# Kernel optimization log

Hardware: AMD Instinct MI355X
Metric: run time of the kernel (lower is better)

The kernel has to match this reference:

```python
import jax, jax.numpy as jnp
import numpy as np

LN_EPS = 1e-5
NEG_INF = -1e38

def _layer_norm(x, g, b):
    mu = x.mean(-1, keepdims=True)
    var = ((x - mu) ** 2).mean(-1, keepdims=True)
    return (x - mu) * jax.lax.rsqrt(var + LN_EPS) * g + b

def _wkv(w, u, k, v):
    # w,u: [C]; k,v: [B,T,C]. Numerically-stable RWKV WKV scan over T.
    B, T, C = k.shape
    kt = jnp.swapaxes(k, 0, 1)  # [T,B,C]
    vt = jnp.swapaxes(v, 0, 1)
    aa0 = jnp.zeros((B, C), k.dtype)
    bb0 = jnp.zeros((B, C), k.dtype)
    pp0 = jnp.full((B, C), NEG_INF, k.dtype)

    def step(carry, inp):
        aa, bb, pp = carry
        kk, vv = inp
        p = jnp.maximum(pp, u + kk)
        e1 = jnp.exp(pp - p)
        e2 = jnp.exp(u + kk - p)
        y = (e1 * aa + e2 * vv) / (e1 + e2)
        p2 = jnp.maximum(pp + w, w + kk)
        e1u = jnp.exp(pp + w - p2)
        e2u = jnp.exp(w + kk - p2)
        aa2 = e1u * aa + e2u * vv
        bb2 = e1u + e2u
        pp2 = p2 + jnp.log(bb2)
        return (aa2, bb2, pp2), y

    _, ys = jax.lax.scan(step, (aa0, bb0, pp0), (kt, vt))
    return jnp.swapaxes(ys, 0, 1)  # [B,T,C]

def _shift(h):
    # x_prev: zero-pad one step at the front (state=None path)
    return jnp.pad(h[:, :-1, :], ((0, 0), (1, 0), (0, 0)))

def setup_inputs() -> dict:
    key = jax.random.key(0)
    B, T, C = 8, 2048, 1024
    ks = jax.random.split(key, 12)
    s = 0.02
    return {
        "x": jax.random.normal(ks[0], (B, T, C), jnp.float32),
        "time_decay": jax.random.normal(ks[1], (C,), jnp.float32) * 0.01,
        "time_first": jax.random.normal(ks[2], (C,), jnp.float32) * 0.01,
        "w_tk": jax.random.normal(ks[3], (C, C), jnp.float32) * s,
        "w_tv": jax.random.normal(ks[4], (C, C), jnp.float32) * s,
        "w_tr": jax.random.normal(ks[5], (C, C), jnp.float32) * s,
        "w_ck": jax.random.normal(ks[6], (C, 4 * C), jnp.float32) * s,
        "w_cv": jax.random.normal(ks[7], (4 * C, C), jnp.float32) * s,
        "w_cr": jax.random.normal(ks[8], (C, C), jnp.float32) * s,
        "ln1_g": jnp.ones((C,), jnp.float32),
        "ln1_b": jnp.zeros((C,), jnp.float32),
        "ln2_g": jnp.ones((C,), jnp.float32),
        "ln2_b": jnp.zeros((C,), jnp.float32),
        "mix_k": jnp.ones((1, 1, C), jnp.float32),
        "mix_v": jnp.ones((1, 1, C), jnp.float32),
        "mix_r": jnp.ones((1, 1, C), jnp.float32),
        "cmix_k": jnp.ones((1, 1, C), jnp.float32),
        "cmix_r": jnp.ones((1, 1, C), jnp.float32),
    }

def reference(x, time_decay, time_first, w_tk, w_tv, w_tr, w_ck, w_cv, w_cr,
              ln1_g, ln1_b, ln2_g, ln2_b, mix_k, mix_v, mix_r, cmix_k, cmix_r):
    # --- time mixing (residual branch 1); dropout is identity at eval ---
    h = _layer_norm(x, ln1_g, ln1_b)
    hp = _shift(h)
    xk = h * mix_k + hp * (1.0 - mix_k)
    xv = h * mix_v + hp * (1.0 - mix_v)
    xr = h * mix_r + hp * (1.0 - mix_r)
    k = xk @ w_tk
    v = xv @ w_tv
    r = jax.nn.sigmoid(xr @ w_tr)
    y = _wkv(time_decay, time_first, k, v)
    x = x + r * y
    # --- channel mixing (residual branch 2) ---
    h2 = _layer_norm(x, ln2_g, ln2_b)
    hp2 = _shift(h2)
    ck = h2 * cmix_k + hp2 * (1.0 - cmix_k)
    cr = h2 * cmix_r + hp2 * (1.0 - cmix_r)
    kk = jnp.square(jax.nn.relu(ck @ w_ck))  # [B,T,4C]
    x = x + jax.nn.sigmoid(cr @ w_cr) * (kk @ w_cv)
    return x
```

## Files before the change

kernel.cpp:

```cpp
#include <hip/hip_runtime.h>
#include <hip/hip_bf16.h>
#include <stdint.h>

#define LN_EPS 1e-5f
#define LNR 8

typedef __attribute__((ext_vector_type(8))) __bf16 bf16x8;
typedef __attribute__((ext_vector_type(8))) short short8;
typedef __attribute__((ext_vector_type(4))) float floatx4;

__device__ __forceinline__ ushort f2bf(float f) {
    __hip_bfloat16 h = __float2bfloat16(f);
    return *reinterpret_cast<ushort*>(&h);
}
__device__ __forceinline__ float bf2f(ushort u) {
    return __builtin_bit_cast(float, ((unsigned int)u) << 16);
}

__device__ __forceinline__ void gload16(const void* g, void* l) {
#if __has_builtin(__builtin_amdgcn_global_load_lds)
    __builtin_amdgcn_global_load_lds(
        (const __attribute__((address_space(1))) unsigned int*)g,
        (__attribute__((address_space(3))) unsigned int*)l, 16, 0, 0);
#else
    *(int4*)l = *(const int4*)g;
#endif
}

#define SBAR __builtin_amdgcn_s_barrier()
#define SCHED0 __builtin_amdgcn_sched_barrier(0)
#define WAIT_LGKM0 asm volatile("s_waitcnt lgkmcnt(0)" ::: "memory")
#define WAIT_VM4 asm volatile("s_waitcnt vmcnt(4)" ::: "memory")
#define WAIT_VM0 asm volatile("s_waitcnt vmcnt(0)" ::: "memory")

#define STAGE_A(h, t)                                                        \
    do {                                                                     \
        ushort* _d = &lds[((((t) & 1) * 2 + 0) * 2 + (h)) * 8192];           \
        const long _o = (long)(h) * 128 * lda + (long)(t) * 64;              \
        gload16(aS0 + _o, _d + tid * 8);                                     \
        gload16(aS1 + _o, _d + (tid + 512) * 8);                             \
    } while (0)
#define STAGE_B(h, t)                                                        \
    do {                                                                     \
        ushort* _d = &lds[((((t) & 1) * 2 + 1) * 2 + (h)) * 8192];           \
        const long _o = (long)(h) * 128 * ldb + (long)(t) * 64;              \
        gload16(bS0 + _o, _d + tid * 8);                                     \
        gload16(bS1 + _o, _d + (tid + 512) * 8);                             \
    } while (0)
#define GEMM_LDA(MB)                                                         \
    _Pragma("unroll") for (int mi = 0; mi < 4; ++mi)                         \
    _Pragma("unroll") for (int ks = 0; ks < 2; ++ks)                         \
        a[mi][ks] = __builtin_bit_cast(                                      \
            bf16x8, *(const short8*)&ldsA[((MB) + mi) * 1024 + ks * 512 + aoff]);
#define GEMM_LDB(NB)                                                         \
    _Pragma("unroll") for (int ni = 0; ni < 2; ++ni)                         \
    _Pragma("unroll") for (int ks = 0; ks < 2; ++ks)                         \
        b[(NB) + ni][ks] = __builtin_bit_cast(                               \
            bf16x8, *(const short8*)&ldsB[((NB) + ni) * 1024 + ks * 512 + boff]);
#define GEMM_MFMA(MB, NB)                                                    \
    __builtin_amdgcn_s_setprio(1);                                           \
    _Pragma("unroll") for (int mi = 0; mi < 4; ++mi)                         \
    _Pragma("unroll") for (int ni = 0; ni < 2; ++ni)                         \
    _Pragma("unroll") for (int ks = 0; ks < 2; ++ks)                         \
        acc[(MB) + mi][(NB) + ni] = __builtin_amdgcn_mfma_f32_16x16x32_bf16( \
            a[mi][ks], b[(NB) + ni][ks], acc[(MB) + mi][(NB) + ni], 0, 0, 0);\
    __builtin_amdgcn_s_setprio(0);

template <int EPI>
__global__ __launch_bounds__(512, 2) void gemm256(
    const ushort* __restrict__ A, const ushort* __restrict__ Bt,
    int K, int lda, int ldb, int ldc,
    float* __restrict__ outF, ushort* __restrict__ outB,
    const float* __restrict__ add0, const ushort* __restrict__ mul0) {
    extern __shared__ ushort lds[];

    const int tid  = threadIdx.x;
    const int lane = tid & 63;
    const int quad = lane >> 4;
    const int l16  = lane & 15;
    const int wv   = tid >> 6;
    const int wmi  = wv >> 2;
    const int wni  = wv & 3;

    const int gx  = gridDim.x;
    const int nwg = gx * gridDim.y;
    int b_ = blockIdx.y * gx + blockIdx.x;
    b_ = (b_ & 7) * (nwg >> 3) + (b_ >> 3);
    const long m0 = (long)(b_ / gx) * 256;
    const long n0 = (long)(b_ % gx) * 256;

    floatx4 acc[8][4];
#pragma unroll
    for (int i = 0; i < 8; ++i)
#pragma unroll
        for (int j = 0; j < 4; ++j) acc[i][j] = (floatx4)0.f;

    const int j1 = tid + 512;
    const int r0 = ((tid >> 7) << 4) + (tid & 15);
    const int c0 = (tid >> 4) & 7;
    const int col0 = (c0 & 3) * 8 + (c0 >> 2) * 32;
    const int r1 = ((j1 >> 7) << 4) + (j1 & 15);
    const int c1 = (j1 >> 4) & 7;
    const int col1 = (c1 & 3) * 8 + (c1 >> 2) * 32;
    const ushort* aS0 = A + (m0 + r0) * (long)lda + col0;
    const ushort* aS1 = A + (m0 + r1) * (long)lda + col1;
    const ushort* bS0 = Bt + (n0 + r0) * (long)ldb + col0;
    const ushort* bS1 = Bt + (n0 + r1) * (long)ldb + col1;

    const int aoff = quad * 128 + l16 * 8;
    const int boff = (wni & 1) * 4096 + quad * 128 + l16 * 8;

    const int NT = K >> 6;

    STAGE_A(0, 0); STAGE_A(1, 0);
    STAGE_B(0, 0); STAGE_B(1, 0);
    if (NT > 1) { STAGE_B(0, 1); STAGE_B(1, 1); WAIT_VM4; }
    else        { WAIT_VM0; }
    SBAR;

    bf16x8 a[4][2], b[4][2];
    for (int kt = 0; kt < NT; ++kt) {
        const int d = kt & 1;
        const ushort* ldsA = &lds[((d * 2 + 0) * 2 + wmi) * 8192];
        const ushort* ldsB = &lds[((d * 2 + 1) * 2 + (wni >> 1)) * 8192];

        GEMM_LDA(0)
        GEMM_LDB(0)
        GEMM_LDB(2)
        if (kt + 1 < NT) { STAGE_A(0, kt + 1); STAGE_A(1, kt + 1); }
        SBAR; WAIT_LGKM0; SCHED0;
        GEMM_MFMA(0, 0)
        GEMM_MFMA(0, 2)
        SCHED0; SBAR;

        GEMM_LDA(4)
        if (kt + 2 < NT) { STAGE_B(0, kt + 2); STAGE_B(1, kt + 2); }
        SBAR; WAIT_LGKM0; SCHED0;
        GEMM_MFMA(4, 0)
        GEMM_MFMA(4, 2)
        SCHED0;
        if (kt < NT - 2) { WAIT_VM4; } else { WAIT_VM0; }
        SBAR;
    }

#pragma unroll
    for (int mi = 0; mi < 8; ++mi) {
#pragma unroll
        for (int ni = 0; ni < 4; ++ni) {
            const long n = n0 + wni * 64 + ni * 16 + l16;
#pragma unroll
            for (int r = 0; r < 4; ++r) {
                const long m = m0 + wmi * 128 + mi * 16 + quad * 4 + r;
                const long idx = m * (long)ldc + n;
                float v = acc[mi][ni][r];
                if constexpr (EPI == 0) {
                    outB[idx] = f2bf(v);
                } else if constexpr (EPI == 1) {
                    outB[idx] = f2bf(1.f / (1.f + __expf(-v)));
                } else if constexpr (EPI == 2) {
                    float t = fmaxf(v, 0.f);
                    outB[idx] = f2bf(t * t);
                } else if constexpr (EPI == 3) {
                    outF[idx] = add0[idx] + bf2f(mul0[idx]) * v;
                }
            }
        }
    }
}

__global__ __launch_bounds__(256) void ln_mix3_b(
    const float* __restrict__ x, const float* __restrict__ g,
    const float* __restrict__ be,
    const float* __restrict__ mx0, const float* __restrict__ mx1,
    const float* __restrict__ mx2,
    ushort* __restrict__ o0, ushort* __restrict__ o1, ushort* __restrict__ o2,
    int T, int C) {
    const long r0 = (long)blockIdx.x * LNR;
    const int tid = threadIdx.x;
    const int i0 = tid * 4;
    const int wv = tid >> 6;
    __shared__ float part[2][4][2];

    const floatx4 gv  = *(const floatx4*)&g[i0];
    const floatx4 bv  = *(const floatx4*)&be[i0];
    const floatx4 mk0 = *(const floatx4*)&mx0[i0];
    const floatx4 mk1 = *(const floatx4*)&mx1[i0];
    const floatx4 mk2 = *(const floatx4*)&mx2[i0];
    const float invC = 1.f / (float)C;

    floatx4 hp = (floatx4)0.f;
    if ((int)(r0 % T) != 0) {
        floatx4 xp = *(const floatx4*)&x[(r0 - 1) * C + i0];
        float s = xp.x + xp.y + xp.z + xp.w;
        float q = xp.x * xp.x + xp.y * xp.y + xp.z * xp.z + xp.w * xp.w;
#pragma unroll
        for (int off = 32; off; off >>= 1) {
            s += __shfl_xor(s, off); q += __shfl_xor(q, off);
        }
        if ((tid & 63) == 0) { part[0][wv][0] = s; part[0][wv][1] = q; }
        __syncthreads();
        s = part[0][0][0] + part[0][1][0] + part[0][2][0] + part[0][3][0];
        q = part[0][0][1] + part[0][1][1] + part[0][2][1] + part[0][3][1];
        float mu = s * invC;
        float rs = rsqrtf(q * invC - mu * mu + LN_EPS);
        hp = (xp - mu) * rs * gv + bv;
        __syncthreads();
    }

    for (int r = 0; r < LNR; ++r) {
        const long row = r0 + r;
        floatx4 xc = *(const floatx4*)&x[row * C + i0];
        float s = xc.x + xc.y + xc.z + xc.w;
        float q = xc.x * xc.x + xc.y * xc.y + xc.z * xc.z + xc.w * xc.w;
#pragma unroll
        for (int off = 32; off; off >>= 1) {
            s += __shfl_xor(s, off); q += __shfl_xor(q, off);
        }
        const int pb = r & 1;
        if ((tid & 63) == 0) { part[pb][wv][0] = s; part[pb][wv][1] = q; }
        __syncthreads();
        s = part[pb][0][0] + part[pb][1][0] + part[pb][2][0] + part[pb][3][0];
        q = part[pb][0][1] + part[pb][1][1] + part[pb][2][1] + part[pb][3][1];
        float mu = s * invC;
        float rs = rsqrtf(q * invC - mu * mu + LN_EPS);
        floatx4 hc = (xc - mu) * rs * gv + bv;

        {
            floatx4 v = hc * mk0 + hp * (1.f - mk0);
            ushort4 pk;
            pk.x = f2bf(v.x); pk.y = f2bf(v.y); pk.z = f2bf(v.z); pk.w = f2bf(v.w);
            *(ushort4*)&o0[row * C + i0] = pk;
        }
        {
            floatx4 v = hc * mk1 + hp * (1.f - mk1);
            ushort4 pk;
            pk.x = f2bf(v.x); pk.y = f2bf(v.y); pk.z = f2bf(v.z); pk.w = f2bf(v.w);
            *(ushort4*)&o1[row * C + i0] = pk;
        }
        {
            floatx4 v = hc * mk2 + hp * (1.f - mk2);
            ushort4 pk;
            pk.x = f2bf(v.x); pk.y = f2bf(v.y); pk.z = f2bf(v.z); pk.w = f2bf(v.w);
            *(ushort4*)&o2[row * C + i0] = pk;
        }
        hp = hc;
    }
}

__global__ __launch_bounds__(256) void ln_mix_add_b(
    const float* __restrict__ x, const ushort* __restrict__ ry,
    const float* __restrict__ g, const float* __restrict__ be,
    const float* __restrict__ mx0, const float* __restrict__ mx1,
    float* __restrict__ outx,
    ushort* __restrict__ o0, ushort* __restrict__ o1, int T, int C) {
    const long r0 = (long)blockIdx.x * LNR;
    const int tid = threadIdx.x;
    const int i0 = tid * 4;
    const int wv = tid >> 6;
    __shared__ float part[2][4][2];

    const floatx4 gv  = *(const floatx4*)&g[i0];
    const floatx4 bv  = *(const floatx4*)&be[i0];
    const floatx4 mk0 = *(const floatx4*)&mx0[i0];
    const floatx4 mk1 = *(const floatx4*)&mx1[i0];
    const float invC = 1.f / (float)C;

    floatx4 hp = (floatx4)0.f;
    if ((int)(r0 % T) != 0) {
        floatx4 xp = *(const floatx4*)&x[(r0 - 1) * C + i0];
        ushort4 rp = *(const ushort4*)&ry[(r0 - 1) * C + i0];
        xp.x += bf2f(rp.x); xp.y += bf2f(rp.y); xp.z += bf2f(rp.z); xp.w += bf2f(rp.w);
        float s = xp.x + xp.y + xp.z + xp.w;
        float q = xp.x * xp.x + xp.y * xp.y + xp.z * xp.z + xp.w * xp.w;
#pragma unroll
        for (int off = 32; off; off >>= 1) {
            s += __shfl_xor(s, off); q += __shfl_xor(q, off);
        }
        if ((tid & 63) == 0) { part[0][wv][0] = s; part[0][wv][1] = q; }
        __syncthreads();
        s = part[0][0][0] + part[0][1][0] + part[0][2][0] + part[0][3][0];
        q = part[0][0][1] + part[0][1][1] + part[0][2][1] + part[0][3][1];
        float mu = s * invC;
        float rs = rsqrtf(q * invC - mu * mu + LN_EPS);
        hp = (xp - mu) * rs * gv + bv;
        __syncthreads();
    }

    for (int r = 0; r < LNR; ++r) {
        const long row = r0 + r;
        floatx4 xc = *(const floatx4*)&x[row * C + i0];
        ushort4 rc = *(const ushort4*)&ry[row * C + i0];
        xc.x += bf2f(rc.x); xc.y += bf2f(rc.y); xc.z += bf2f(rc.z); xc.w += bf2f(rc.w);
        *(floatx4*)&outx[row * C + i0] = xc;

        float s = xc.x + xc.y + xc.z + xc.w;
        float q = xc.x * xc.x + xc.y * xc.y + xc.z * xc.z + xc.w * xc.w;
#pragma unroll
        for (int off = 32; off; off >>= 1) {
            s += __shfl_xor(s, off); q += __shfl_xor(q, off);
        }
        const int pb = r & 1;
        if ((tid & 63) == 0) { part[pb][wv][0] = s; part[pb][wv][1] = q; }
        __syncthreads();
        s = part[pb][0][0] + part[pb][1][0] + part[pb][2][0] + part[pb][3][0];
        q = part[pb][0][1] + part[pb][1][1] + part[pb][2][1] + part[pb][3][1];
        float mu = s * invC;
        float rs = rsqrtf(q * invC - mu * mu + LN_EPS);
        floatx4 hc = (xc - mu) * rs * gv + bv;

        {
            floatx4 v = hc * mk0 + hp * (1.f - mk0);
            ushort4 pk;
            pk.x = f2bf(v.x); pk.y = f2bf(v.y); pk.z = f2bf(v.z); pk.w = f2bf(v.w);
            *(ushort4*)&o0[row * C + i0] = pk;
        }
        {
            floatx4 v = hc * mk1 + hp * (1.f - mk1);
            ushort4 pk;
            pk.x = f2bf(v.x); pk.y = f2bf(v.y); pk.z = f2bf(v.z); pk.w = f2bf(v.w);
            *(ushort4*)&o1[row * C + i0] = pk;
        }
        hp = hc;
    }
}


__global__ __launch_bounds__(256) void wkv_pp_local(
    const float* __restrict__ w, const ushort* __restrict__ k,
    float* __restrict__ pp_loc, int C, int L) {
    const int g = blockIdx.x * 256 + threadIdx.x;
    const int c = g % C;
    const long seg = g / C;
    const float L2E = 1.4426950408889634f;
    const float w2 = w[c] * L2E;
    const ushort* kp = k + seg * L * C + c;
    float pp = -1e38f;
    for (int j = 0; j < L; ++j) {
        float kk = bf2f(kp[(long)j * C]) * L2E;
        float ppw = pp + w2;
        float wk = w2 + kk;
        float p2 = fmaxf(ppw, wk);
        pp = p2 + log2f(exp2f(ppw - p2) + exp2f(wk - p2));
    }
    pp_loc[g] = pp;
}

__global__ __launch_bounds__(256) void wkv_pp_compose(
    const float* __restrict__ w, const float* __restrict__ pp_loc,
    float* __restrict__ pp_in, int C, int SEG, int L) {
    const int g = blockIdx.x * 256 + threadIdx.x;
    const int c = g % C;
    const long b = g / C;
    const float wL = w[c] * 1.4426950408889634f * (float)L;
    float pp = -1e38f;
    for (int s = 0; s < SEG; ++s) {
        const long idx = (b * SEG + s) * C + c;
        pp_in[idx] = pp;
        float lhs = pp + wL;
        float rhs = pp_loc[idx];
        float m = fmaxf(lhs, rhs);
        pp = m + log2f(exp2f(lhs - m) + exp2f(rhs - m));
    }
}

__global__ __launch_bounds__(256) void wkv_ab_local(
    const float* __restrict__ w, const ushort* __restrict__ k,
    const ushort* __restrict__ v, const float* __restrict__ pp_in,
    float* __restrict__ alpha, float* __restrict__ beta, int C, int L) {
    const int g = blockIdx.x * 256 + threadIdx.x;
    const int c = g % C;
    const long seg = g / C;
    const float L2E = 1.4426950408889634f;
    const float w2 = w[c] * L2E;
    const ushort* kp = k + seg * L * C + c;
    const ushort* vp = v + seg * L * C + c;
    float pp = pp_in[g];
    float al = 1.f, be = 0.f;
    for (int j = 0; j < L; ++j) {
        float kk = bf2f(kp[(long)j * C]) * L2E;
        float vv = bf2f(vp[(long)j * C]);
        float ppw = pp + w2;
        float wk = w2 + kk;
        float p2 = fmaxf(ppw, wk);
        float e1u = exp2f(ppw - p2);
        float e2u = exp2f(wk - p2);
        al *= e1u;
        be = e1u * be + e2u * vv;
        pp = p2 + log2f(e1u + e2u);
    }
    alpha[g] = al;
    beta[g] = be;
}

__global__ __launch_bounds__(256) void wkv_aa_compose(
    const float* __restrict__ alpha, const float* __restrict__ beta,
    float* __restrict__ aa_in, int C, int SEG) {
    const int g = blockIdx.x * 256 + threadIdx.x;
    const int c = g % C;
    const long b = g / C;
    float aa = 0.f;
    for (int s = 0; s < SEG; ++s) {
        const long idx = (b * SEG + s) * C + c;
        aa_in[idx] = aa;
        aa = alpha[idx] * aa + beta[idx];
    }
    (void)c;
}

__global__ __launch_bounds__(256) void wkv_emit(
    const float* __restrict__ w, const float* __restrict__ u,
    const ushort* __restrict__ k, const ushort* __restrict__ v,
    const ushort* __restrict__ r, const float* __restrict__ aa_in,
    const float* __restrict__ pp_in, ushort* __restrict__ ry, int C, int L) {
    const int g = blockIdx.x * 256 + threadIdx.x;
    const int c = g % C;
    const long seg = g / C;
    const float L2E = 1.4426950408889634f;
    const float w2 = w[c] * L2E;
    const float u2 = u[c] * L2E;
    const long base = seg * L * C + c;
    const ushort* kp = k + base;
    const ushort* vp = v + base;
    const ushort* rp = r + base;
    ushort* op = ry + base;
    float aa = aa_in[g];
    float pp = pp_in[g];
    for (int j = 0; j < L; ++j) {
        const long o = (long)j * C;
        float kk = bf2f(kp[o]) * L2E;
        float vv = bf2f(vp[o]);
        float uk = u2 + kk;
        float p = fmaxf(pp, uk);
        float e1 = exp2f(pp - p);
        float e2 = exp2f(uk - p);
        float y = __fdividef(e1 * aa + e2 * vv, e1 + e2);
        op[o] = f2bf(bf2f(rp[o]) * y);
        float ppw = pp + w2;
        float wk = w2 + kk;
        float p2 = fmaxf(ppw, wk);
        float e1u = exp2f(ppw - p2);
        float e2u = exp2f(wk - p2);
        aa = e1u * aa + e2u * vv;
        pp = p2 + log2f(e1u + e2u);
    }
}

__global__ __launch_bounds__(256) void transpose_bf16(
    const float* __restrict__ in, ushort* __restrict__ out, int K, int N) {
    __shared__ float tile[32][33];
    const int tx = threadIdx.x, ty = threadIdx.y;
    const long k0 = (long)blockIdx.y * 32, n0 = (long)blockIdx.x * 32;
#pragma unroll
    for (int i = 0; i < 4; i++)
        tile[ty + i * 8][tx] = in[(k0 + ty + i * 8) * N + n0 + tx];
    __syncthreads();
#pragma unroll
    for (int i = 0; i < 4; i++)
        out[(n0 + ty + i * 8) * K + k0 + tx] = f2bf(tile[tx][ty + i * 8]);
}

__global__ __launch_bounds__(256) void transpose4_bf16(
    const float* __restrict__ a0, const float* __restrict__ a1,
    const float* __restrict__ a2, const float* __restrict__ a3,
    ushort* __restrict__ b0, ushort* __restrict__ b1,
    ushort* __restrict__ b2, ushort* __restrict__ b3, int K, int N) {
    __shared__ float tile[32][33];
    const int z = blockIdx.z;
    const float* in = (z == 0) ? a0 : (z == 1) ? a1 : (z == 2) ? a2 : a3;
    ushort* out = (z == 0) ? b0 : (z == 1) ? b1 : (z == 2) ? b2 : b3;
    const int tx = threadIdx.x, ty = threadIdx.y;
    const long k0 = (long)blockIdx.y * 32, n0 = (long)blockIdx.x * 32;
#pragma unroll
    for (int i = 0; i < 4; i++)
        tile[ty + i * 8][tx] = in[(k0 + ty + i * 8) * N + n0 + tx];
    __syncthreads();
#pragma unroll
    for (int i = 0; i < 4; i++)
        out[(n0 + ty + i * 8) * K + k0 + tx] = f2bf(tile[tx][ty + i * 8]);
}

extern "C" void kernel_launch(void* const* d_in, const int* in_sizes, int n_in,
                              void* d_out, int out_size, void* d_ws, size_t ws_size,
                              hipStream_t stream) {
    const float* x      = (const float*)d_in[0];
    const float* tdecay = (const float*)d_in[1];
    const float* tfirst = (const float*)d_in[2];
    const float* w_tk   = (const float*)d_in[3];
    const float* w_tv   = (const float*)d_in[4];
    const float* w_tr   = (const float*)d_in[5];
    const float* w_ck   = (const float*)d_in[6];
    const float* w_cv   = (const float*)d_in[7];
    const float* w_cr   = (const float*)d_in[8];
    const float* ln1g   = (const float*)d_in[9];
    const float* ln1b   = (const float*)d_in[10];
    const float* ln2g   = (const float*)d_in[11];
    const float* ln2b   = (const float*)d_in[12];
    const float* mixk   = (const float*)d_in[13];
    const float* mixv   = (const float*)d_in[14];
    const float* mixr   = (const float*)d_in[15];
    const float* cmixk  = (const float*)d_in[16];
    const float* cmixr  = (const float*)d_in[17];
    float* out = (float*)d_out;

    const int C  = in_sizes[1];
    const long M = (long)in_sizes[0] / C;
    const int T  = 2048;
    const int B  = (int)(M / T);
    const int H  = 2 * C;
    const int SEG = 64;
    const int L  = T / SEG;
    const int NSEG = B * SEG;

    static bool s_attr = []() {
        (void)hipFuncSetAttribute((const void*)gemm256<0>,
                                  hipFuncAttributeMaxDynamicSharedMemorySize, 131072);
        (void)hipFuncSetAttribute((const void*)gemm256<1>,
                                  hipFuncAttributeMaxDynamicSharedMemorySize, 131072);
        (void)hipFuncSetAttribute((const void*)gemm256<2>,
                                  hipFuncAttributeMaxDynamicSharedMemorySize, 131072);
        (void)hipFuncSetAttribute((const void*)gemm256<3>,
                                  hipFuncAttributeMaxDynamicSharedMemorySize, 131072);
        return true;
    }();
    (void)s_attr;
    const int SMEM = 131072;

    const size_t MBy = 1024ull * 1024ull;
    char* w8 = (char*)d_ws;
    ushort* wT_tk  = (ushort*)(w8 + 0 * MBy);
    ushort* wT_tv  = (ushort*)(w8 + 2 * MBy);
    ushort* wT_tr  = (ushort*)(w8 + 4 * MBy);
    ushort* wT_cr  = (ushort*)(w8 + 6 * MBy);
    ushort* wT_ck  = (ushort*)(w8 + 8 * MBy);
    ushort* wT_cv0 = (ushort*)(w8 + 16 * MBy);
    ushort* wT_cv1 = (ushort*)(w8 + 20 * MBy);
    ushort* xk     = (ushort*)(w8 + 24 * MBy);
    ushort* xv     = (ushort*)(w8 + 56 * MBy);
    ushort* xr     = (ushort*)(w8 + 88 * MBy);
    ushort* kbuf   = (ushort*)(w8 + 120 * MBy);
    ushort* vbuf   = (ushort*)(w8 + 152 * MBy);
    ushort* rbuf   = (ushort*)(w8 + 24 * MBy);
    float*  pp_loc = (float*)(w8 + 56 * MBy);
    float*  pp_in  = (float*)(w8 + 58 * MBy);
    float*  alpha  = (float*)(w8 + 60 * MBy);
    float*  beta   = (float*)(w8 + 62 * MBy);
    float*  aa_in  = (float*)(w8 + 64 * MBy);
    ushort* ry     = (ushort*)(w8 + 88 * MBy);
    ushort* ck     = (ushort*)(w8 + 120 * MBy);
    ushort* cr     = (ushort*)(w8 + 152 * MBy);
    ushort* scr    = (ushort*)(w8 + 24 * MBy);
    ushort* kkbuf  = (ushort*)(w8 + 56 * MBy);

    dim3 tb(32, 8);
    transpose4_bf16<<<dim3(C / 32, C / 32, 4), tb, 0, stream>>>(
        w_tk, w_tv, w_tr, w_cr, wT_tk, wT_tv, wT_tr, wT_cr, C, C);
    transpose_bf16<<<dim3(4 * C / 32, C / 32), tb, 0, stream>>>(w_ck, wT_ck, C, 4 * C);
    transpose_bf16<<<dim3(C / 32, H / 32), tb, 0, stream>>>(w_cv, wT_cv0, H, C);
    transpose_bf16<<<dim3(C / 32, H / 32), tb, 0, stream>>>(w_cv + (long)H * C, wT_cv1, H, C);

    ln_mix3_b<<<(int)(M / LNR), 256, 0, stream>>>(x, ln1g, ln1b, mixk, mixv, mixr,
                                                  xk, xv, xr, T, C);

    dim3 g256(C / 256, (int)(M / 256));
    gemm256<0><<<g256, 512, SMEM, stream>>>(xk, wT_tk, C, C, C, C,
                                            nullptr, kbuf, nullptr, nullptr);
    gemm256<0><<<g256, 512, SMEM, stream>>>(xv, wT_tv, C, C, C, C,
                                            nullptr, vbuf, nullptr, nullptr);
    gemm256<1><<<g256, 512, SMEM, stream>>>(xr, wT_tr, C, C, C, C,
                                            nullptr, rbuf, nullptr, nullptr);

    const int segthreads = NSEG * C;
    wkv_pp_local<<<segthreads / 256, 256, 0, stream>>>(tdecay, kbuf, pp_loc, C, L);
    wkv_pp_compose<<<(B * C) / 256, 256, 0, stream>>>(tdecay, pp_loc, pp_in, C, SEG, L);
    wkv_ab_local<<<segthreads / 256, 256, 0, stream>>>(tdecay, kbuf, vbuf, pp_in,
                                                       alpha, beta, C, L);
    wkv_aa_compose<<<(B * C) / 256, 256, 0, stream>>>(alpha, beta, aa_in, C, SEG);
    wkv_emit<<<segthreads / 256, 256, 0, stream>>>(tdecay, tfirst, kbuf, vbuf, rbuf,
                                                   aa_in, pp_in, ry, C, L);

    ln_mix_add_b<<<(int)(M / LNR), 256, 0, stream>>>(x, ry, ln2g, ln2b, cmixk, cmixr,
                                                     out, ck, cr, T, C);

    gemm256<1><<<g256, 512, SMEM, stream>>>(cr, wT_cr, C, C, C, C,
                                            nullptr, scr, nullptr, nullptr);

    for (int h = 0; h < 2; ++h) {
        const ushort* wck_h = wT_ck + (long)h * H * C;
        const ushort* wcv_h = (h == 0) ? wT_cv0 : wT_cv1;
        gemm256<2><<<dim3(H / 256, (int)(M / 256)), 512, SMEM, stream>>>(
            ck, wck_h, C, C, C, H, nullptr, kkbuf, nullptr, nullptr);
        gemm256<3><<<g256, 512, SMEM, stream>>>(
            kkbuf, wcv_h, H, H, H, C, out, nullptr, out, scr);
    }
}
```

Measured before the change: 867.4 us.

## Restructure GEMM mainloop into four-stage ring with K-tile 32

The bf16 GEMM kernel now stages A and B together in K-slices of 32 into a four-buffer LDS ring, keeping three slices in flight. Each iteration does one barrier and 32 MFMAs. This replaces the earlier double-buffered K=64 scheme, which staged A and B at separate points and synchronised with several barriers per tile. The goal is deeper prefetch and less barrier overhead. In exchange there are twice as many loop iterations and waitcnt points, and a different LDS layout that could cause bank conflicts.

```diff
diff --git a/kernel.cpp b/kernel.cpp
--- a/kernel.cpp
+++ b/kernel.cpp
@@ -30,41 +30,19 @@
 #define SBAR __builtin_amdgcn_s_barrier()
 #define SCHED0 __builtin_amdgcn_sched_barrier(0)
 #define WAIT_LGKM0 asm volatile("s_waitcnt lgkmcnt(0)" ::: "memory")
+#define WAIT_VM8 asm volatile("s_waitcnt vmcnt(8)" ::: "memory")
 #define WAIT_VM4 asm volatile("s_waitcnt vmcnt(4)" ::: "memory")
 #define WAIT_VM0 asm volatile("s_waitcnt vmcnt(0)" ::: "memory")
 
-#define STAGE_A(h, t)                                                        \
+#define STAGE_T(t)                                                           \
     do {                                                                     \
-        ushort* _d = &lds[((((t) & 1) * 2 + 0) * 2 + (h)) * 8192];           \
-        const long _o = (long)(h) * 128 * lda + (long)(t) * 64;              \
-        gload16(aS0 + _o, _d + tid * 8);                                     \
-        gload16(aS1 + _o, _d + (tid + 512) * 8);                             \
+        ushort* _d = &lds[((t) & 3) * 16384];                                \
+        const long _ko = (long)(t) * 32;                                     \
+        gload16(aS0 + _ko, _d + tid * 8);                                    \
+        gload16(aS1 + _ko, _d + (tid + 512) * 8);                            \
+        gload16(bS0 + _ko, _d + 8192 + tid * 8);                             \
+        gload16(bS1 + _ko, _d + 8192 + (tid + 512) * 8);                     \
     } while (0)
-#define STAGE_B(h, t)                                                        \
-    do {                                                                     \
-        ushort* _d = &lds[((((t) & 1) * 2 + 1) * 2 + (h)) * 8192];           \
-        const long _o = (long)(h) * 128 * ldb + (long)(t) * 64;              \
-        gload16(bS0 + _o, _d + tid * 8);                                     \
-        gload16(bS1 + _o, _d + (tid + 512) * 8);                             \
-    } while (0)
-#define GEMM_LDA(MB)                                                         \
-    _Pragma("unroll") for (int mi = 0; mi < 4; ++mi)                         \
-    _Pragma("unroll") for (int ks = 0; ks < 2; ++ks)                         \
-        a[mi][ks] = __builtin_bit_cast(                                      \
-            bf16x8, *(const short8*)&ldsA[((MB) + mi) * 1024 + ks * 512 + aoff]);
-#define GEMM_LDB(NB)                                                         \
-    _Pragma("unroll") for (int ni = 0; ni < 2; ++ni)                         \
-    _Pragma("unroll") for (int ks = 0; ks < 2; ++ks)                         \
-        b[(NB) + ni][ks] = __builtin_bit_cast(                               \
-            bf16x8, *(const short8*)&ldsB[((NB) + ni) * 1024 + ks * 512 + boff]);
-#define GEMM_MFMA(MB, NB)                                                    \
-    __builtin_amdgcn_s_setprio(1);                                           \
-    _Pragma("unroll") for (int mi = 0; mi < 4; ++mi)                         \
-    _Pragma("unroll") for (int ni = 0; ni < 2; ++ni)                         \
-    _Pragma("unroll") for (int ks = 0; ks < 2; ++ks)                         \
-        acc[(MB) + mi][(NB) + ni] = __builtin_amdgcn_mfma_f32_16x16x32_bf16( \
-            a[mi][ks], b[(NB) + ni][ks], acc[(MB) + mi][(NB) + ni], 0, 0, 0);\
-    __builtin_amdgcn_s_setprio(0);
 
 template <int EPI>
 __global__ __launch_bounds__(512, 2) void gemm256(
@@ -96,50 +74,53 @@
         for (int j = 0; j < 4; ++j) acc[i][j] = (floatx4)0.f;
 
     const int j1 = tid + 512;
-    const int r0 = ((tid >> 7) << 4) + (tid & 15);
-    const int c0 = (tid >> 4) & 7;
-    const int col0 = (c0 & 3) * 8 + (c0 >> 2) * 32;
-    const int r1 = ((j1 >> 7) << 4) + (j1 & 15);
-    const int c1 = (j1 >> 4) & 7;
-    const int col1 = (c1 & 3) * 8 + (c1 >> 2) * 32;
-    const ushort* aS0 = A + (m0 + r0) * (long)lda + col0;
-    const ushort* aS1 = A + (m0 + r1) * (long)lda + col1;
-    const ushort* bS0 = Bt + (n0 + r0) * (long)ldb + col0;
-    const ushort* bS1 = Bt + (n0 + r1) * (long)ldb + col1;
+    const int r0 = ((tid >> 6) << 4) + (tid & 15);
+    const int c0 = ((tid >> 4) & 3) * 8;
+    const int r1 = ((j1 >> 6) << 4) + (j1 & 15);
+    const int c1 = ((j1 >> 4) & 3) * 8;
+    const ushort* aS0 = A + (m0 + r0) * (long)lda + c0;
+    const ushort* aS1 = A + (m0 + r1) * (long)lda + c1;
+    const ushort* bS0 = Bt + (n0 + r0) * (long)ldb + c0;
+    const ushort* bS1 = Bt + (n0 + r1) * (long)ldb + c1;
 
     const int aoff = quad * 128 + l16 * 8;
-    const int boff = (wni & 1) * 4096 + quad * 128 + l16 * 8;
-
-    const int NT = K >> 6;
-
-    STAGE_A(0, 0); STAGE_A(1, 0);
-    STAGE_B(0, 0); STAGE_B(1, 0);
-    if (NT > 1) { STAGE_B(0, 1); STAGE_B(1, 1); WAIT_VM4; }
-    else        { WAIT_VM0; }
+
+    const int NK = K >> 5;
+
+    STAGE_T(0); STAGE_T(1); STAGE_T(2);
+    WAIT_VM8;
     SBAR;
 
-    bf16x8 a[4][2], b[4][2];
-    for (int kt = 0; kt < NT; ++kt) {
-        const int d = kt & 1;
-        const ushort* ldsA = &lds[((d * 2 + 0) * 2 + wmi) * 8192];
-        const ushort* ldsB = &lds[((d * 2 + 1) * 2 + (wni >> 1)) * 8192];
-
-        GEMM_LDA(0)
-        GEMM_LDB(0)
-        GEMM_LDB(2)
-        if (kt + 1 < NT) { STAGE_A(0, kt + 1); STAGE_A(1, kt + 1); }
-        SBAR; WAIT_LGKM0; SCHED0;
-        GEMM_MFMA(0, 0)
-        GEMM_MFMA(0, 2)
-        SCHED0; SBAR;
-
-        GEMM_LDA(4)
-        if (kt + 2 < NT) { STAGE_B(0, kt + 2); STAGE_B(1, kt + 2); }
-        SBAR; WAIT_LGKM0; SCHED0;
-        GEMM_MFMA(4, 0)
-        GEMM_MFMA(4, 2)
+    bf16x8 a[8], b[4];
+    for (int kt = 0; kt < NK; ++kt) {
+        const ushort* ldsA = &lds[(kt & 3) * 16384];
+        const ushort* ldsB = ldsA + 8192;
+
+#pragma unroll
+        for (int mi = 0; mi < 8; ++mi)
+            a[mi] = __builtin_bit_cast(
+                bf16x8, *(const short8*)&ldsA[(wmi * 8 + mi) * 512 + aoff]);
+#pragma unroll
+        for (int ni = 0; ni < 4; ++ni)
+            b[ni] = __builtin_bit_cast(
+                bf16x8, *(const short8*)&ldsB[(wni * 4 + ni) * 512 + aoff]);
+
+        if (kt + 3 < NK) STAGE_T(kt + 3);
+
+        WAIT_LGKM0; SCHED0;
+        __builtin_amdgcn_s_setprio(1);
+#pragma unroll
+        for (int mi = 0; mi < 8; ++mi)
+#pragma unroll
+            for (int ni = 0; ni < 4; ++ni)
+                acc[mi][ni] = __builtin_amdgcn_mfma_f32_16x16x32_bf16(
+                    a[mi], b[ni], acc[mi][ni], 0, 0, 0);
+        __builtin_amdgcn_s_setprio(0);
         SCHED0;
-        if (kt < NT - 2) { WAIT_VM4; } else { WAIT_VM0; }
+
+        if (kt + 3 < NK)       { WAIT_VM8; }
+        else if (kt + 3 == NK) { WAIT_VM4; }
+        else                   { WAIT_VM0; }
         SBAR;
     }
 
```

After: 906.5 us. 1.05x slower.
